# Optimization experiments

Hardware: AMD Instinct MI355X
Metric: run time of the kernel (lower is better)

The kernel has to match this reference:

```python
import jax, jax.numpy as jnp
import numpy as np
from jax import lax

WINDOW_SIZE = 11
SIGMA = 1.5
DATA_RANGE = 1.0


def _gaussian_window(channels):
    coords = jnp.arange(WINDOW_SIZE, dtype=jnp.float32) - WINDOW_SIZE // 2
    g = jnp.exp(-coords ** 2 / (2.0 * SIGMA ** 2))
    g = g / g.sum()
    w2d = jnp.outer(g, g)
    w2d = w2d / w2d.sum()
    # depthwise kernel: (C, 1, K, K) in OIHW with feature_group_count=C
    return jnp.broadcast_to(w2d, (channels, 1, WINDOW_SIZE, WINDOW_SIZE))


def _dwconv(x, window, channels):
    pad = WINDOW_SIZE // 2
    return lax.conv_general_dilated(
        x, window,
        window_strides=(1, 1),
        padding=[(pad, pad), (pad, pad)],
        dimension_numbers=('NCHW', 'OIHW', 'NCHW'),
        feature_group_count=channels,
    )


def setup_inputs() -> dict:
    key = jax.random.key(0)
    k1, k2 = jax.random.split(key)
    B, C, H, W = 16, 3, 512, 512
    x = jax.random.uniform(k1, (B, C, H, W), dtype=jnp.float32)
    y = jax.random.uniform(k2, (B, C, H, W), dtype=jnp.float32)
    return {"x": x, "y": y}


def reference(x, y):
    channels = x.shape[1]
    window = _gaussian_window(channels)
    mu_x = _dwconv(x, window, channels)
    mu_y = _dwconv(y, window, channels)
    mu_x2 = mu_x * mu_x
    mu_y2 = mu_y * mu_y
    mu_xy = mu_x * mu_y
    sigma_x2 = _dwconv(x * x, window, channels) - mu_x2
    sigma_y2 = _dwconv(y * y, window, channels) - mu_y2
    sigma_xy = _dwconv(x * y, window, channels) - mu_xy
    c1 = (0.01 * DATA_RANGE) ** 2
    c2 = (0.03 * DATA_RANGE) ** 2
    ssim_map = (2 * mu_xy + c1) * (2 * sigma_xy + c2) / (
        (mu_x2 + mu_y2 + c1) * (sigma_x2 + sigma_y2 + c2) + 1e-08)
    per_image = ssim_map.mean(axis=(1, 2, 3))
    return 1.0 - per_image.mean()
```

## Files before the change

### kernel.cpp

```cpp
#include <hip/hip_runtime.h>
#include <math.h>


#define IMG_W 512
#define IMG_H 512
#define PLANES 48
#define TX 64
#define TY 32
#define RAD 5
#define NT 256
#define GDX (IMG_W / TX)
#define GDY (IMG_H / TY)
#define NBLK (GDX * GDY * PLANES)

#define SROWS 48
#define HSTR  56
#define INVW  0.26601181f
#define GC2   0.32059890f

typedef _Float16 h2 __attribute__((ext_vector_type(2)));
typedef _Float16 h4 __attribute__((ext_vector_type(4)));
typedef _Float16 h8 __attribute__((ext_vector_type(8)));
typedef float f32x4 __attribute__((ext_vector_type(4)));

__device__ __forceinline__ float exp2_fast(float a) {
#if __has_builtin(__builtin_amdgcn_exp2f)
    return __builtin_amdgcn_exp2f(a);
#else
    return exp2f(a);
#endif
}

__device__ __forceinline__ float wbandf(int idx) {
    const float fd = (float)(idx - 5);
    const float g = exp2_fast(-(fd * fd) * GC2) * INVW;
    return ((unsigned)idx <= 10u) ? g : 0.f;
}

__device__ __forceinline__ h2 pkrtz(float a, float b) {
    auto t = __builtin_amdgcn_cvt_pkrtz(a, b);
    h2 r;
    __builtin_memcpy(&r, &t, sizeof(r));
    return r;
}

__device__ __forceinline__ h4 pack4(f32x4 a) {
    const h2 lo = pkrtz(a[0], a[1]), hi = pkrtz(a[2], a[3]);
    h4 v;
    v[0] = lo.x; v[1] = lo.y; v[2] = hi.x; v[3] = hi.y;
    return v;
}

template<bool INTERIOR>
__device__ __forceinline__ void load_sd(const float* __restrict__ xp,
                                        const float* __restrict__ yp,
                                        int gr, int gc, h8& sA, h8& dA)
{
    const float4 z4 = make_float4(0.f, 0.f, 0.f, 0.f);
    float4 xa = z4, xb = z4, ya = z4, yb = z4;
    if (INTERIOR || (unsigned)gr < (unsigned)IMG_H) {
        const float* rx = xp + (size_t)gr * IMG_W;
        const float* ry = yp + (size_t)gr * IMG_W;
        if (INTERIOR || (unsigned)gc < (unsigned)IMG_W) {
            xa = *(const float4*)(rx + gc);
            ya = *(const float4*)(ry + gc);
        }
        if (INTERIOR || (unsigned)(gc + 4) < (unsigned)IMG_W) {
            xb = *(const float4*)(rx + gc + 4);
            yb = *(const float4*)(ry + gc + 4);
        }
    }
    const h2 xh0 = pkrtz(xa.x, xa.y), xh1 = pkrtz(xa.z, xa.w);
    const h2 xh2 = pkrtz(xb.x, xb.y), xh3 = pkrtz(xb.z, xb.w);
    const h2 yh0 = pkrtz(ya.x, ya.y), yh1 = pkrtz(ya.z, ya.w);
    const h2 yh2 = pkrtz(yb.x, yb.y), yh3 = pkrtz(yb.z, yb.w);
    const h2 s0 = xh0 + yh0, s1 = xh1 + yh1, s2 = xh2 + yh2, s3 = xh3 + yh3;
    const h2 d0 = xh0 - yh0, d1 = xh1 - yh1, d2 = xh2 - yh2, d3 = xh3 - yh3;
    sA[0] = s0.x; sA[1] = s0.y; sA[2] = s1.x; sA[3] = s1.y;
    sA[4] = s2.x; sA[5] = s2.y; sA[6] = s3.x; sA[7] = s3.y;
    dA[0] = d0.x; dA[1] = d0.y; dA[2] = d1.x; dA[3] = d1.y;
    dA[4] = d2.x; dA[5] = d2.y; dA[6] = d3.x; dA[7] = d3.y;
}

template<bool INTERIOR>
__device__ __forceinline__ void hconv_all(
    const float* __restrict__ xp, const float* __restrict__ yp,
    int R0, int gcol, int fc, int q, int c0, h8 whB,
    _Float16* __restrict__ Ht)
{
    const f32x4 zz = {0.f, 0.f, 0.f, 0.f};
    #pragma unroll
    for (int i0 = 0; i0 < SROWS; i0 += 16) {
        h8 sA, dA;
        load_sd<INTERIOR>(xp, yp, R0 - RAD + i0 + fc, gcol, sA, dA);
        const h8 s2A = sA * sA;
        const h8 d2A = dA * dA;
        const f32x4 hS  = __builtin_amdgcn_mfma_f32_16x16x32_f16(sA,  whB, zz, 0, 0, 0);
        const f32x4 hD  = __builtin_amdgcn_mfma_f32_16x16x32_f16(dA,  whB, zz, 0, 0, 0);
        const f32x4 hS2 = __builtin_amdgcn_mfma_f32_16x16x32_f16(s2A, whB, zz, 0, 0, 0);
        const f32x4 hD2 = __builtin_amdgcn_mfma_f32_16x16x32_f16(d2A, whB, zz, 0, 0, 0);
        const int hoff = (c0 + fc) * HSTR + i0 + 4 * q;
        *(h4*)&Ht[0 * TX * HSTR + hoff] = pack4(hS);
        *(h4*)&Ht[1 * TX * HSTR + hoff] = pack4(hD);
        *(h4*)&Ht[2 * TX * HSTR + hoff] = pack4(hS2);
        *(h4*)&Ht[3 * TX * HSTR + hoff] = pack4(hD2);
    }
}

__global__ __launch_bounds__(NT, 5) void ssim_tile_kernel(
    const float* __restrict__ x, const float* __restrict__ y,
    float* __restrict__ partials)
{
    __shared__ __align__(16) _Float16 Ht[4 * TX * HSTR];
    __shared__ float wave_sums[NT / 64];

    const int tid = threadIdx.x;
    const int l   = tid & 63, wid = tid >> 6;
    const int q   = l >> 4,  fc  = l & 15;

    float s2w = 0.f;
    #pragma unroll
    for (int k = 0; k <= 10; ++k) s2w += (float)(_Float16)wbandf(k);
    const float cv = 1.f / (s2w * s2w);

    h8 whB, wvA;
    #pragma unroll
    for (int e = 0; e < 8; ++e) whB[e] = (_Float16)wbandf(8 * q + e - fc - 3);
    #pragma unroll
    for (int e = 0; e < 5; ++e) wvA[e] = whB[e + 3];
    #pragma unroll
    for (int e = 5; e < 8; ++e) wvA[e] = (_Float16)wbandf(8 * q + e - fc);

    const int plane = blockIdx.z;
    const float* __restrict__ xp = x + (size_t)plane * IMG_H * IMG_W;
    const float* __restrict__ yp = y + (size_t)plane * IMG_H * IMG_W;
    const int C0 = blockIdx.x * TX;
    const int R0 = blockIdx.y * TY;
    const int c0 = 16 * wid;
    const int gcol = C0 + c0 - 8 + 8 * q;

    const bool interior =
        (blockIdx.x >= 1) && (blockIdx.x <= GDX - 2) &&
        (blockIdx.y >= 1) && (blockIdx.y <= GDY - 2);

    if (interior) hconv_all<true >(xp, yp, R0, gcol, fc, q, c0, whB, Ht);
    else          hconv_all<false>(xp, yp, R0, gcol, fc, q, c0, whB, Ht);


    const f32x4 zz = {0.f, 0.f, 0.f, 0.f};
    float local = 0.f;
    #pragma unroll
    for (int m = 0; m < TY / 16; ++m) {
        const int boff = (c0 + fc) * HSTR + 16 * m + 8 * q;
        const f32x4 aS  = __builtin_amdgcn_mfma_f32_16x16x32_f16(
            wvA, *(const h8*)&Ht[0 * TX * HSTR + boff], zz, 0, 0, 0);
        const f32x4 aD  = __builtin_amdgcn_mfma_f32_16x16x32_f16(
            wvA, *(const h8*)&Ht[1 * TX * HSTR + boff], zz, 0, 0, 0);
        const f32x4 aS2 = __builtin_amdgcn_mfma_f32_16x16x32_f16(
            wvA, *(const h8*)&Ht[2 * TX * HSTR + boff], zz, 0, 0, 0);
        const f32x4 aD2 = __builtin_amdgcn_mfma_f32_16x16x32_f16(
            wvA, *(const h8*)&Ht[3 * TX * HSTR + boff], zz, 0, 0, 0);
        #pragma unroll
        for (int r = 0; r < 4; ++r) {
            const float mS = aS[r]  * cv, mD = aD[r]  * cv;
            const float eS = aS2[r] * cv, eD = aD2[r] * cv;
            const float ms2 = mS * mS, md2 = mD * mD;
            const float Pm = 0.5f * (ms2 - md2);
            const float Qm = 0.5f * (ms2 + md2);
            const float Pe = 0.5f * (eS - eD);
            const float Qe = 0.5f * (eS + eD);
            const float c1 = 1e-4f, c2 = 9e-4f;
            const float num = (Pm + c1) * (Pe - Pm + c2);
            const float den = (Qm + c1) * (Qe - Qm + c2) + 1e-8f;
            local += num * __builtin_amdgcn_rcpf(den);
        }
    }

    #pragma unroll
    for (int off = 32; off > 0; off >>= 1)
        local += __shfl_down(local, off, 64);
    if (l == 0) wave_sums[wid] = local;
    __syncthreads();
    if (tid == 0) {
        const float s = wave_sums[0] + wave_sums[1] + wave_sums[2] + wave_sums[3];
        const int bid = blockIdx.x + GDX * (blockIdx.y + GDY * blockIdx.z);
        partials[bid] = s;
    }
}

__global__ __launch_bounds__(NT) void ssim_finalize_kernel(
    const float* __restrict__ partials, float* __restrict__ out)
{
    const int tid = threadIdx.x;
    double s = 0.0;
    #pragma unroll 4
    for (int i = tid; i < NBLK; i += NT) s += (double)partials[i];
    #pragma unroll
    for (int off = 32; off > 0; off >>= 1)
        s += __shfl_down(s, off, 64);
    __shared__ double ws_[NT / 64];
    const int lane = tid & 63, wv = tid >> 6;
    if (lane == 0) ws_[wv] = s;
    __syncthreads();
    if (tid == 0) {
        const double t = ws_[0] + ws_[1] + ws_[2] + ws_[3];
        const double n = (double)PLANES * IMG_H * IMG_W;
        out[0] = (float)(1.0 - t / n);
    }
}

extern "C" void kernel_launch(void* const* d_in, const int* in_sizes, int n_in,
                              void* d_out, int out_size, void* d_ws, size_t ws_size,
                              hipStream_t stream)
{
    const float* x = (const float*)d_in[0];
    const float* y = (const float*)d_in[1];
    float* out = (float*)d_out;
    float* partials = (float*)d_ws;

    dim3 grid(GDX, GDY, PLANES);
    ssim_tile_kernel<<<grid, NT, 0, stream>>>(x, y, partials);
    ssim_finalize_kernel<<<1, NT, 0, stream>>>(partials, out);
}
```

Baseline: 137.5 us.

## Stream taller tiles through a 3-slot ring buffer with prefetched buffer loads

Each block now covers 128 rows instead of 32 and walks down the tile in 16-row chunks. The horizontally convolved chunks sit in a 3-slot LDS ring, and raw buffer loads for chunks two ahead are issued into registers while the current vertical MFMA pass runs. The taller tile cuts the redundant halo-row reads and overlaps global loads with compute. Out-of-bounds rows and columns are zeroed by the buffer range check instead of an interior/edge template split. In exchange the kernel needs more registers and its launch-bounds occupancy hint drops from 5 to 4, leaving fewer blocks in total.

```diff
diff --git a/kernel.cpp b/kernel.cpp
--- a/kernel.cpp
+++ b/kernel.cpp
@@ -6,15 +6,18 @@
 #define IMG_H 512
 #define PLANES 48
 #define TX 64
-#define TY 32
+#define TYS 128
 #define RAD 5
 #define NT 256
 #define GDX (IMG_W / TX)
-#define GDY (IMG_H / TY)
+#define GDY (IMG_H / TYS)
 #define NBLK (GDX * GDY * PLANES)
-
-#define SROWS 48
-#define HSTR  56
+#define NCH 9
+#define NCV 8
+#define CSTRH 56
+#define PSTRH 3584
+#define NUMREC (IMG_W * IMG_H * 4)
+#define CHSTEP (16 * IMG_W * 4)
 #define INVW  0.26601181f
 #define GC2   0.32059890f
 
@@ -22,6 +25,16 @@
 typedef _Float16 h4 __attribute__((ext_vector_type(4)));
 typedef _Float16 h8 __attribute__((ext_vector_type(8)));
 typedef float f32x4 __attribute__((ext_vector_type(4)));
+typedef int i32x4 __attribute__((ext_vector_type(4)));
+
+__device__ f32x4 buf_ld_x4(i32x4 srsrc, int voffset, int soffset, int aux)
+    __asm("llvm.amdgcn.raw.buffer.load.v4f32");
+
+__device__ __forceinline__ i32x4 make_srd(const float* p) {
+    union { i32x4 v; struct { const float* p; unsigned rng; unsigned cfg; } s; } u;
+    u.s.p = p; u.s.rng = NUMREC; u.s.cfg = 0x00020000u;
+    return u.v;
+}
 
 __device__ __forceinline__ float exp2_fast(float a) {
 #if __has_builtin(__builtin_amdgcn_exp2f)
@@ -51,72 +64,67 @@
     return v;
 }
 
-template<bool INTERIOR>
-__device__ __forceinline__ void load_sd(const float* __restrict__ xp,
-                                        const float* __restrict__ yp,
-                                        int gr, int gc, h8& sA, h8& dA)
-{
-    const float4 z4 = make_float4(0.f, 0.f, 0.f, 0.f);
-    float4 xa = z4, xb = z4, ya = z4, yb = z4;
-    if (INTERIOR || (unsigned)gr < (unsigned)IMG_H) {
-        const float* rx = xp + (size_t)gr * IMG_W;
-        const float* ry = yp + (size_t)gr * IMG_W;
-        if (INTERIOR || (unsigned)gc < (unsigned)IMG_W) {
-            xa = *(const float4*)(rx + gc);
-            ya = *(const float4*)(ry + gc);
-        }
-        if (INTERIOR || (unsigned)(gc + 4) < (unsigned)IMG_W) {
-            xb = *(const float4*)(rx + gc + 4);
-            yb = *(const float4*)(ry + gc + 4);
-        }
-    }
-    const h2 xh0 = pkrtz(xa.x, xa.y), xh1 = pkrtz(xa.z, xa.w);
-    const h2 xh2 = pkrtz(xb.x, xb.y), xh3 = pkrtz(xb.z, xb.w);
-    const h2 yh0 = pkrtz(ya.x, ya.y), yh1 = pkrtz(ya.z, ya.w);
-    const h2 yh2 = pkrtz(yb.x, yb.y), yh3 = pkrtz(yb.z, yb.w);
+__device__ __forceinline__ void hconv_chunk(
+    f32x4 xa, f32x4 xb, f32x4 ya, f32x4 yb, h8 whB,
+    _Float16* wp)
+{
+    const f32x4 zz = {0.f, 0.f, 0.f, 0.f};
+    const h2 xh0 = pkrtz(xa[0], xa[1]), xh1 = pkrtz(xa[2], xa[3]);
+    const h2 xh2 = pkrtz(xb[0], xb[1]), xh3 = pkrtz(xb[2], xb[3]);
+    const h2 yh0 = pkrtz(ya[0], ya[1]), yh1 = pkrtz(ya[2], ya[3]);
+    const h2 yh2 = pkrtz(yb[0], yb[1]), yh3 = pkrtz(yb[2], yb[3]);
     const h2 s0 = xh0 + yh0, s1 = xh1 + yh1, s2 = xh2 + yh2, s3 = xh3 + yh3;
     const h2 d0 = xh0 - yh0, d1 = xh1 - yh1, d2 = xh2 - yh2, d3 = xh3 - yh3;
+    h8 sA, dA;
     sA[0] = s0.x; sA[1] = s0.y; sA[2] = s1.x; sA[3] = s1.y;
     sA[4] = s2.x; sA[5] = s2.y; sA[6] = s3.x; sA[7] = s3.y;
     dA[0] = d0.x; dA[1] = d0.y; dA[2] = d1.x; dA[3] = d1.y;
     dA[4] = d2.x; dA[5] = d2.y; dA[6] = d3.x; dA[7] = d3.y;
-}
-
-template<bool INTERIOR>
-__device__ __forceinline__ void hconv_all(
-    const float* __restrict__ xp, const float* __restrict__ yp,
-    int R0, int gcol, int fc, int q, int c0, h8 whB,
-    _Float16* __restrict__ Ht)
-{
-    const f32x4 zz = {0.f, 0.f, 0.f, 0.f};
-    #pragma unroll
-    for (int i0 = 0; i0 < SROWS; i0 += 16) {
-        h8 sA, dA;
-        load_sd<INTERIOR>(xp, yp, R0 - RAD + i0 + fc, gcol, sA, dA);
-        const h8 s2A = sA * sA;
-        const h8 d2A = dA * dA;
-        const f32x4 hS  = __builtin_amdgcn_mfma_f32_16x16x32_f16(sA,  whB, zz, 0, 0, 0);
-        const f32x4 hD  = __builtin_amdgcn_mfma_f32_16x16x32_f16(dA,  whB, zz, 0, 0, 0);
-        const f32x4 hS2 = __builtin_amdgcn_mfma_f32_16x16x32_f16(s2A, whB, zz, 0, 0, 0);
-        const f32x4 hD2 = __builtin_amdgcn_mfma_f32_16x16x32_f16(d2A, whB, zz, 0, 0, 0);
-        const int hoff = (c0 + fc) * HSTR + i0 + 4 * q;
-        *(h4*)&Ht[0 * TX * HSTR + hoff] = pack4(hS);
-        *(h4*)&Ht[1 * TX * HSTR + hoff] = pack4(hD);
-        *(h4*)&Ht[2 * TX * HSTR + hoff] = pack4(hS2);
-        *(h4*)&Ht[3 * TX * HSTR + hoff] = pack4(hD2);
-    }
-}
-
-__global__ __launch_bounds__(NT, 5) void ssim_tile_kernel(
+    const h8 s2A = sA * sA;
+    const h8 d2A = dA * dA;
+    const f32x4 hS  = __builtin_amdgcn_mfma_f32_16x16x32_f16(sA,  whB, zz, 0, 0, 0);
+    const f32x4 hD  = __builtin_amdgcn_mfma_f32_16x16x32_f16(dA,  whB, zz, 0, 0, 0);
+    const f32x4 hS2 = __builtin_amdgcn_mfma_f32_16x16x32_f16(s2A, whB, zz, 0, 0, 0);
+    const f32x4 hD2 = __builtin_amdgcn_mfma_f32_16x16x32_f16(d2A, whB, zz, 0, 0, 0);
+    *(h4*)(wp + 0 * PSTRH) = pack4(hS);
+    *(h4*)(wp + 1 * PSTRH) = pack4(hD);
+    *(h4*)(wp + 2 * PSTRH) = pack4(hS2);
+    *(h4*)(wp + 3 * PSTRH) = pack4(hD2);
+}
+
+__global__ __launch_bounds__(NT, 4) void ssim_tile_kernel(
     const float* __restrict__ x, const float* __restrict__ y,
     float* __restrict__ partials)
 {
-    __shared__ __align__(16) _Float16 Ht[4 * TX * HSTR];
+    __shared__ __align__(16) _Float16 Ht[4 * TX * CSTRH];
     __shared__ float wave_sums[NT / 64];
 
     const int tid = threadIdx.x;
-    const int l   = tid & 63, wid = tid >> 6;
-    const int q   = l >> 4,  fc  = l & 15;
+    const int l = tid & 63, wid = tid >> 6;
+    const int q = l >> 4, fc = l & 15;
+    const int qh = q >> 1, ql = q & 1;
+
+    const int plane = blockIdx.z;
+    const i32x4 srdx = make_srd(x + (size_t)plane * IMG_H * IMG_W);
+    const i32x4 srdy = make_srd(y + (size_t)plane * IMG_H * IMG_W);
+    const int C0 = blockIdx.x * TX;
+    const int R0 = blockIdx.y * TYS;
+    const int c0 = 16 * wid;
+    const int col = c0 + fc;
+    const int gcol = C0 + c0 - 8 + 8 * q;
+    const int gr0 = R0 - RAD + fc;
+    int voff = ((unsigned)gcol < (unsigned)IMG_W)
+             ? ((gr0 << 11) + (gcol << 2)) : 0x60000000;
+
+    f32x4 LXA[3], LXB[3], LYA[3], LYB[3];
+    #pragma unroll
+    for (int c = 0; c < 3; ++c) {
+        LXA[c] = buf_ld_x4(srdx, voff, 0, 0);
+        LXB[c] = buf_ld_x4(srdx, voff, 16, 0);
+        LYA[c] = buf_ld_x4(srdy, voff, 0, 0);
+        LYB[c] = buf_ld_x4(srdy, voff, 16, 0);
+        voff += CHSTEP;
+    }
 
     float s2w = 0.f;
     #pragma unroll
@@ -131,35 +139,36 @@
     #pragma unroll
     for (int e = 5; e < 8; ++e) wvA[e] = (_Float16)wbandf(8 * q + e - fc);
 
-    const int plane = blockIdx.z;
-    const float* __restrict__ xp = x + (size_t)plane * IMG_H * IMG_W;
-    const float* __restrict__ yp = y + (size_t)plane * IMG_H * IMG_W;
-    const int C0 = blockIdx.x * TX;
-    const int R0 = blockIdx.y * TY;
-    const int c0 = 16 * wid;
-    const int gcol = C0 + c0 - 8 + 8 * q;
-
-    const bool interior =
-        (blockIdx.x >= 1) && (blockIdx.x <= GDX - 2) &&
-        (blockIdx.y >= 1) && (blockIdx.y <= GDY - 2);
-
-    if (interior) hconv_all<true >(xp, yp, R0, gcol, fc, q, c0, whB, Ht);
-    else          hconv_all<false>(xp, yp, R0, gcol, fc, q, c0, whB, Ht);
-
+    _Float16* const hw = Ht + col * CSTRH + 4 * q;
+    const int rb = col * CSTRH + 8 * ql;
+
+    hconv_chunk(LXA[0], LXB[0], LYA[0], LYB[0], whB, hw + 0 * 16);
+    hconv_chunk(LXA[1], LXB[1], LYA[1], LYB[1], whB, hw + 1 * 16);
 
     const f32x4 zz = {0.f, 0.f, 0.f, 0.f};
     float local = 0.f;
-    #pragma unroll
-    for (int m = 0; m < TY / 16; ++m) {
-        const int boff = (c0 + fc) * HSTR + 16 * m + 8 * q;
+    int vslot = qh;
+    #pragma unroll
+    for (int m = 0; m < NCV; ++m) {
+        if (m + 3 < NCH) {
+            LXA[m % 3] = buf_ld_x4(srdx, voff, 0, 0);
+            LXB[m % 3] = buf_ld_x4(srdx, voff, 16, 0);
+            LYA[m % 3] = buf_ld_x4(srdy, voff, 0, 0);
+            LYB[m % 3] = buf_ld_x4(srdy, voff, 16, 0);
+            voff += CHSTEP;
+        }
+
+        const _Float16* rp = Ht + rb + vslot * 16;
         const f32x4 aS  = __builtin_amdgcn_mfma_f32_16x16x32_f16(
-            wvA, *(const h8*)&Ht[0 * TX * HSTR + boff], zz, 0, 0, 0);
+            wvA, *(const h8*)(rp + 0 * PSTRH), zz, 0, 0, 0);
         const f32x4 aD  = __builtin_amdgcn_mfma_f32_16x16x32_f16(
-            wvA, *(const h8*)&Ht[1 * TX * HSTR + boff], zz, 0, 0, 0);
+            wvA, *(const h8*)(rp + 1 * PSTRH), zz, 0, 0, 0);
         const f32x4 aS2 = __builtin_amdgcn_mfma_f32_16x16x32_f16(
-            wvA, *(const h8*)&Ht[2 * TX * HSTR + boff], zz, 0, 0, 0);
+            wvA, *(const h8*)(rp + 2 * PSTRH), zz, 0, 0, 0);
         const f32x4 aD2 = __builtin_amdgcn_mfma_f32_16x16x32_f16(
-            wvA, *(const h8*)&Ht[3 * TX * HSTR + boff], zz, 0, 0, 0);
+            wvA, *(const h8*)(rp + 3 * PSTRH), zz, 0, 0, 0);
+        vslot = (vslot == 2) ? 0 : vslot + 1;
+
         #pragma unroll
         for (int r = 0; r < 4; ++r) {
             const float mS = aS[r]  * cv, mD = aD[r]  * cv;
@@ -174,6 +183,11 @@
             const float den = (Qm + c1) * (Qe - Qm + c2) + 1e-8f;
             local += num * __builtin_amdgcn_rcpf(den);
         }
+
+        if (m + 2 < NCH)
+            hconv_chunk(LXA[(m + 2) % 3], LXB[(m + 2) % 3],
+                        LYA[(m + 2) % 3], LYB[(m + 2) % 3],
+                        whB, hw + ((m + 2) % 3) * 16);
     }
 
     #pragma unroll
```

After: 132.9 us. 1.04x faster.
